# Performance work log

Measured on AMD Instinct MI355X. Metric: run time of the kernel, lower is better.

## Reference

```python
import jax, jax.numpy as jnp
import numpy as np

B, N = 32, 14            # hardcoded in the torch module
IN_F, OUT_F, H = 1024, 1024, 4
ALPHA = 0.2              # leaky relu negative slope
NEG = -9e15


def setup_inputs() -> dict:
    key = jax.random.key(0)
    ks = jax.random.split(key, 6)
    # xavier-uniform-ish scales (exact init values don't affect correctness testing)
    x = jax.random.normal(ks[0], (B, N, IN_F), dtype=jnp.float32)
    adj = jax.random.normal(ks[1], (B, N, N), dtype=jnp.float32)
    W = jax.random.normal(ks[2], (H, B, IN_F, OUT_F), dtype=jnp.float32) * (1.414 / np.sqrt(IN_F))
    a = jax.random.normal(ks[3], (H, B, 2 * OUT_F, 1), dtype=jnp.float32) * (1.414 / np.sqrt(2 * OUT_F))
    fc_w = jax.random.normal(ks[4], (H, OUT_F, N * OUT_F), dtype=jnp.float32) * (1.0 / np.sqrt(N * OUT_F))
    fc_b = jnp.zeros((H, OUT_F), dtype=jnp.float32)
    return {"x": x, "adj": adj, "W": W, "a": a, "fc_w": fc_w, "fc_b": fc_b}


def reference(x, adj, W, a, fc_w, fc_b):
    # Wh: [H, B, N, OUT_F]
    Wh = jnp.einsum('bni,hbio->hbno', x, W)
    a1 = a[:, :, :OUT_F, 0]   # [H, B, OUT_F]
    a2 = a[:, :, OUT_F:, 0]   # [H, B, OUT_F]
    Wh1 = jnp.einsum('hbno,hbo->hbn', Wh, a1)  # [H, B, N]
    Wh2 = jnp.einsum('hbno,hbo->hbn', Wh, a2)  # [H, B, N]
    e = jax.nn.leaky_relu(Wh1[..., :, None] + Wh2[..., None, :], negative_slope=ALPHA)  # [H,B,N,N]
    att = jnp.where(adj[None] > 0, e, NEG)
    # torch F.softmax(attention, dim=1) on [B,N,N] -> axis=2 here (first node axis)
    att = jax.nn.softmax(att, axis=2)
    # dropout p=0 (eval) -> no-op
    h_prime = jnp.einsum('hbnm,hbmo->hbno', att, Wh).reshape(H, B, N * OUT_F)
    out_h = jnp.einsum('hbf,hof->hbo', h_prime, fc_w) + fc_b[:, None, :]  # [H, B, OUT_F]
    out = out_h.sum(axis=0)                                              # [B, OUT_F]
    return jax.nn.log_softmax(out, axis=1)
```

## Files before the change

kernel.cpp:

```cpp
#include <hip/hip_runtime.h>
#include <hip/hip_bf16.h>

#define ALPHA 0.2f
#define NEGV  -9000000000000000.0f

typedef __attribute__((ext_vector_type(8))) short bf16x8;
typedef __attribute__((ext_vector_type(4))) float f32x4;

__device__ __forceinline__ short f2b(float f) {
  unsigned u = __float_as_uint(f);
  unsigned r = (u + 0x7FFFu + ((u >> 16) & 1u)) >> 16;
  return (short)r;
}

__global__ __launch_bounds__(256) void k1_wh(const float* __restrict__ x,
                                             const float* __restrict__ W,
                                             float* __restrict__ Wh) {
  int blk = blockIdx.x;
  int kc = blk & 3;
  int hb = blk >> 2;
  int b  = hb & 31;
  int t  = threadIdx.x;
  __shared__ float xs[14][256];
  int i0 = kc * 256;
  const float* xb = x + (size_t)b * 14 * 1024 + i0;
  #pragma unroll
  for (int n = 0; n < 14; ++n) xs[n][t] = xb[n * 1024 + t];
  __syncthreads();

  const float* Wp = W + ((size_t)hb * 1024 + i0) * 1024 + 4 * t;
  float4 acc[14];
  #pragma unroll
  for (int n = 0; n < 14; ++n) acc[n] = make_float4(0.f, 0.f, 0.f, 0.f);

  for (int ii = 0; ii < 256; ii += 4) {
    float4 w0 = *(const float4*)(Wp + (size_t)(ii + 0) * 1024);
    float4 w1 = *(const float4*)(Wp + (size_t)(ii + 1) * 1024);
    float4 w2 = *(const float4*)(Wp + (size_t)(ii + 2) * 1024);
    float4 w3 = *(const float4*)(Wp + (size_t)(ii + 3) * 1024);
    #pragma unroll
    for (int n = 0; n < 14; ++n) {
      float4 xn = *(const float4*)&xs[n][ii];
      acc[n].x += xn.x * w0.x + xn.y * w1.x + xn.z * w2.x + xn.w * w3.x;
      acc[n].y += xn.x * w0.y + xn.y * w1.y + xn.z * w2.y + xn.w * w3.y;
      acc[n].z += xn.x * w0.z + xn.y * w1.z + xn.z * w2.z + xn.w * w3.z;
      acc[n].w += xn.x * w0.w + xn.y * w1.w + xn.z * w2.w + xn.w * w3.w;
    }
  }

  float* dst = Wh + (size_t)hb * 14336 + 4 * t;
  #pragma unroll
  for (int n = 0; n < 14; ++n) {
    atomicAdd(dst + n * 1024 + 0, acc[n].x);
    atomicAdd(dst + n * 1024 + 1, acc[n].y);
    atomicAdd(dst + n * 1024 + 2, acc[n].z);
    atomicAdd(dst + n * 1024 + 3, acc[n].w);
  }
}

__global__ __launch_bounds__(64) void k2_att(const float* __restrict__ Wh,
                                             const float* __restrict__ adj,
                                             const float* __restrict__ a,
                                             float* __restrict__ att) {
  int hb = blockIdx.x;
  int b  = hb & 31;
  int l  = threadIdx.x;
  __shared__ float wh1s[14], wh2s[14];
  const float* whp = Wh + (size_t)hb * 14336;
  const float* a1  = a + (size_t)hb * 2048;
  const float* a2  = a1 + 1024;

  for (int n = 0; n < 14; ++n) {
    float p1 = 0.f, p2 = 0.f;
    #pragma unroll
    for (int j = 0; j < 16; ++j) {
      int o = l + 64 * j;
      float wv = whp[n * 1024 + o];
      p1 += wv * a1[o];
      p2 += wv * a2[o];
    }
    #pragma unroll
    for (int s = 32; s >= 1; s >>= 1) {
      p1 += __shfl_xor(p1, s);
      p2 += __shfl_xor(p2, s);
    }
    if (l == 0) { wh1s[n] = p1; wh2s[n] = p2; }
  }
  __syncthreads();

  if (l < 14) {
    int m = l;
    const float* adjb = adj + b * 196;
    float col[14];
    float mx = -1e30f;
    #pragma unroll
    for (int n = 0; n < 14; ++n) {
      float e = wh1s[n] + wh2s[m];
      e = (e > 0.f) ? e : ALPHA * e;
      e = (adjb[n * 14 + m] > 0.f) ? e : NEGV;
      col[n] = e;
      mx = fmaxf(mx, e);
    }
    float s = 0.f;
    #pragma unroll
    for (int n = 0; n < 14; ++n) { col[n] = expf(col[n] - mx); s += col[n]; }
    float inv = 1.f / s;
    #pragma unroll
    for (int n = 0; n < 14; ++n) att[hb * 196 + n * 14 + m] = col[n] * inv;
  }
}

__global__ __launch_bounds__(128) void k3_hprime(const float* __restrict__ Wh,
                                                 const float* __restrict__ att,
                                                 float* __restrict__ hp) {
  int blk = blockIdx.x;
  int hb = blk >> 1, oc = blk & 1;
  int t = threadIdx.x;
  __shared__ float att_s[196];
  for (int idx = t; idx < 196; idx += 128) att_s[idx] = att[hb * 196 + idx];
  __syncthreads();

  int o4 = oc * 512 + 4 * t;
  const float* whp = Wh + (size_t)hb * 14336;
  float4 acc[14];
  #pragma unroll
  for (int n = 0; n < 14; ++n) acc[n] = make_float4(0.f, 0.f, 0.f, 0.f);
  #pragma unroll
  for (int m = 0; m < 14; ++m) {
    float4 wm = *(const float4*)(whp + m * 1024 + o4);
    #pragma unroll
    for (int n = 0; n < 14; ++n) {
      float anm = att_s[n * 14 + m];
      acc[n].x += anm * wm.x;
      acc[n].y += anm * wm.y;
      acc[n].z += anm * wm.z;
      acc[n].w += anm * wm.w;
    }
  }
  float* dst = hp + (size_t)hb * 14336 + o4;
  #pragma unroll
  for (int n = 0; n < 14; ++n) *(float4*)(dst + n * 1024) = acc[n];
}

__global__ __launch_bounds__(256) void k4_fc(const float* __restrict__ hp,
                                             const float* __restrict__ fcw,
                                             float* __restrict__ oacc) {
  int blk = blockIdx.x;
  int kc = blk & 7;
  int oc = (blk >> 3) & 15;
  int h  = blk >> 7;
  int t = threadIdx.x;
  int lane = t & 63, w = t >> 6;
  int mw = w & 1, nw = w >> 1;
  __shared__ __align__(16) short As[32][272];
  __shared__ __align__(16) short Bs[64][272];
  const int o0 = oc * 64;
  const size_t hpb = (size_t)h * 32 * 14336;
  const size_t fwb = (size_t)h * 1024 * 14336;
  f32x4 c0 = {0.f, 0.f, 0.f, 0.f};
  f32x4 c1 = {0.f, 0.f, 0.f, 0.f};

  for (int tt = 0; tt < 7; ++tt) {
    int f0 = kc * 1792 + tt * 256;
    #pragma unroll
    for (int p = 0; p < 8; ++p) {
      int f4 = p * 256 + t;
      int row = f4 >> 6, c4 = f4 & 63;
      float4 wv = *(const float4*)(hp + hpb + (size_t)row * 14336 + f0 + 4 * c4);
      short4 s4 = make_short4(f2b(wv.x), f2b(wv.y), f2b(wv.z), f2b(wv.w));
      *(short4*)&As[row][4 * c4] = s4;
    }
    #pragma unroll
    for (int p = 0; p < 16; ++p) {
      int f4 = p * 256 + t;
      int row = f4 >> 6, c4 = f4 & 63;
      float4 wv = *(const float4*)(fcw + fwb + (size_t)(o0 + row) * 14336 + f0 + 4 * c4);
      short4 s4 = make_short4(f2b(wv.x), f2b(wv.y), f2b(wv.z), f2b(wv.w));
      *(short4*)&Bs[row][4 * c4] = s4;
    }
    __syncthreads();
    #pragma unroll
    for (int ks = 0; ks < 8; ++ks) {
      bf16x8 af = *(const bf16x8*)&As[mw * 16 + (lane & 15)][ks * 32 + (lane >> 4) * 8];
      bf16x8 b0 = *(const bf16x8*)&Bs[nw * 32 + (lane & 15)][ks * 32 + (lane >> 4) * 8];
      bf16x8 b1 = *(const bf16x8*)&Bs[nw * 32 + 16 + (lane & 15)][ks * 32 + (lane >> 4) * 8];
      c0 = __builtin_amdgcn_mfma_f32_16x16x32_bf16(af, b0, c0, 0, 0, 0);
      c1 = __builtin_amdgcn_mfma_f32_16x16x32_bf16(af, b1, c1, 0, 0, 0);
    }
    __syncthreads();
  }
  int br   = mw * 16 + (lane >> 4) * 4;
  int ocol = o0 + nw * 32 + (lane & 15);
  #pragma unroll
  for (int r = 0; r < 4; ++r) {
    atomicAdd(&oacc[(br + r) * 1024 + ocol],      c0[r]);
    atomicAdd(&oacc[(br + r) * 1024 + ocol + 16], c1[r]);
  }
}

__global__ __launch_bounds__(256) void k5_lsm(const float* __restrict__ oacc,
                                              const float* __restrict__ fcb,
                                              float* __restrict__ out) {
  int b = blockIdx.x, t = threadIdx.x;
  int lane = t & 63, wid = t >> 6;
  __shared__ float redm[4], reds[4];
  float v[4];
  float mx = -1e30f;
  #pragma unroll
  for (int j = 0; j < 4; ++j) {
    int o = t + 256 * j;
    float val = oacc[b * 1024 + o] + fcb[o] + fcb[1024 + o] + fcb[2048 + o] + fcb[3072 + o];
    v[j] = val;
    mx = fmaxf(mx, val);
  }
  #pragma unroll
  for (int s = 32; s >= 1; s >>= 1) mx = fmaxf(mx, __shfl_xor(mx, s));
  if (lane == 0) redm[wid] = mx;
  __syncthreads();
  mx = fmaxf(fmaxf(redm[0], redm[1]), fmaxf(redm[2], redm[3]));
  float sm = 0.f;
  #pragma unroll
  for (int j = 0; j < 4; ++j) sm += expf(v[j] - mx);
  #pragma unroll
  for (int s = 32; s >= 1; s >>= 1) sm += __shfl_xor(sm, s);
  if (lane == 0) reds[wid] = sm;
  __syncthreads();
  sm = reds[0] + reds[1] + reds[2] + reds[3];
  float lse = mx + logf(sm);
  #pragma unroll
  for (int j = 0; j < 4; ++j) {
    int o = t + 256 * j;
    out[b * 1024 + o] = v[j] - lse;
  }
}

extern "C" void kernel_launch(void* const* d_in, const int* in_sizes, int n_in,
                              void* d_out, int out_size, void* d_ws, size_t ws_size,
                              hipStream_t stream) {
  const float* x   = (const float*)d_in[0];
  const float* adj = (const float*)d_in[1];
  const float* W   = (const float*)d_in[2];
  const float* a   = (const float*)d_in[3];
  const float* fcw = (const float*)d_in[4];
  const float* fcb = (const float*)d_in[5];
  float* out = (float*)d_out;

  char* ws = (char*)d_ws;
  float* Wh  = (float*)(ws);
  float* att = (float*)(ws + 7340032);
  float* hp  = (float*)(ws + 7440384);
  float* oac = (float*)(ws + 14780416);

  hipMemsetAsync(Wh, 0, 7340032, stream);
  hipMemsetAsync(oac, 0, 131072, stream);

  k1_wh<<<512, 256, 0, stream>>>(x, W, Wh);
  k2_att<<<128, 64, 0, stream>>>(Wh, adj, a, att);
  k3_hprime<<<256, 128, 0, stream>>>(Wh, att, hp);
  k4_fc<<<512, 256, 0, stream>>>(hp, fcw, oac);
  k5_lsm<<<32, 256, 0, stream>>>(oac, fcb, out);
}
```

Before: 962.9 us.

## Replace split-K atomics with partial buffers and separate reduction passes

The k1 and k4 split-K kernels now write partial results to separate workspace slices instead of doing fp32 atomicAdd. A new k1b_red kernel and an extended k5 loop sum those partials. The two hipMemsetAsync calls are dropped. k2_att now uses two waves to compute the per-node attention dot products. This removes atomic contention and memset launches, at the cost of about 29 MB of extra partial traffic and one more kernel launch.

```diff
diff --git a/kernel.cpp b/kernel.cpp
--- a/kernel.cpp
+++ b/kernel.cpp
@@ -15,7 +15,7 @@
 
 __global__ __launch_bounds__(256) void k1_wh(const float* __restrict__ x,
                                              const float* __restrict__ W,
-                                             float* __restrict__ Wh) {
+                                             float* __restrict__ Whp) {
   int blk = blockIdx.x;
   int kc = blk & 3;
   int hb = blk >> 2;
@@ -48,29 +48,41 @@
     }
   }
 
-  float* dst = Wh + (size_t)hb * 14336 + 4 * t;
-  #pragma unroll
-  for (int n = 0; n < 14; ++n) {
-    atomicAdd(dst + n * 1024 + 0, acc[n].x);
-    atomicAdd(dst + n * 1024 + 1, acc[n].y);
-    atomicAdd(dst + n * 1024 + 2, acc[n].z);
-    atomicAdd(dst + n * 1024 + 3, acc[n].w);
-  }
-}
-
-__global__ __launch_bounds__(64) void k2_att(const float* __restrict__ Wh,
-                                             const float* __restrict__ adj,
-                                             const float* __restrict__ a,
-                                             float* __restrict__ att) {
+  float* dst = Whp + (size_t)kc * 1835008 + (size_t)hb * 14336 + 4 * t;
+  #pragma unroll
+  for (int n = 0; n < 14; ++n) *(float4*)(dst + n * 1024) = acc[n];
+}
+
+__global__ __launch_bounds__(256) void k1b_red(const float* __restrict__ p,
+                                               float* __restrict__ Wh) {
+  size_t idx = ((size_t)blockIdx.x * 256 + threadIdx.x) * 4;
+  const size_t S = 1835008;
+  float4 a = *(const float4*)(p + idx);
+  float4 b = *(const float4*)(p + S + idx);
+  float4 c = *(const float4*)(p + 2 * S + idx);
+  float4 d = *(const float4*)(p + 3 * S + idx);
+  a.x += b.x + c.x + d.x;
+  a.y += b.y + c.y + d.y;
+  a.z += b.z + c.z + d.z;
+  a.w += b.w + c.w + d.w;
+  *(float4*)(Wh + idx) = a;
+}
+
+__global__ __launch_bounds__(128) void k2_att(const float* __restrict__ Wh,
+                                              const float* __restrict__ adj,
+                                              const float* __restrict__ a,
+                                              float* __restrict__ att) {
   int hb = blockIdx.x;
   int b  = hb & 31;
-  int l  = threadIdx.x;
+  int t  = threadIdx.x;
+  int l  = t & 63, w = t >> 6;
   __shared__ float wh1s[14], wh2s[14];
   const float* whp = Wh + (size_t)hb * 14336;
   const float* a1  = a + (size_t)hb * 2048;
   const float* a2  = a1 + 1024;
 
-  for (int n = 0; n < 14; ++n) {
+  for (int nn = 0; nn < 7; ++nn) {
+    int n = w * 7 + nn;
     float p1 = 0.f, p2 = 0.f;
     #pragma unroll
     for (int j = 0; j < 16; ++j) {
@@ -88,8 +100,8 @@
   }
   __syncthreads();
 
-  if (l < 14) {
-    int m = l;
+  if (t < 14) {
+    int m = t;
     const float* adjb = adj + b * 196;
     float col[14];
     float mx = -1e30f;
@@ -144,7 +156,7 @@
 
 __global__ __launch_bounds__(256) void k4_fc(const float* __restrict__ hp,
                                              const float* __restrict__ fcw,
-                                             float* __restrict__ oacc) {
+                                             float* __restrict__ oaccp) {
   int blk = blockIdx.x;
   int kc = blk & 7;
   int oc = (blk >> 3) & 15;
@@ -189,16 +201,17 @@
     }
     __syncthreads();
   }
+  float* op = oaccp + (size_t)(kc * 4 + h) * 32768;
   int br   = mw * 16 + (lane >> 4) * 4;
   int ocol = o0 + nw * 32 + (lane & 15);
   #pragma unroll
   for (int r = 0; r < 4; ++r) {
-    atomicAdd(&oacc[(br + r) * 1024 + ocol],      c0[r]);
-    atomicAdd(&oacc[(br + r) * 1024 + ocol + 16], c1[r]);
-  }
-}
-
-__global__ __launch_bounds__(256) void k5_lsm(const float* __restrict__ oacc,
+    op[(br + r) * 1024 + ocol]      = c0[r];
+    op[(br + r) * 1024 + ocol + 16] = c1[r];
+  }
+}
+
+__global__ __launch_bounds__(256) void k5_lsm(const float* __restrict__ oaccp,
                                               const float* __restrict__ fcb,
                                               float* __restrict__ out) {
   int b = blockIdx.x, t = threadIdx.x;
@@ -209,7 +222,9 @@
   #pragma unroll
   for (int j = 0; j < 4; ++j) {
     int o = t + 256 * j;
-    float val = oacc[b * 1024 + o] + fcb[o] + fcb[1024 + o] + fcb[2048 + o] + fcb[3072 + o];
+    float val = fcb[o] + fcb[1024 + o] + fcb[2048 + o] + fcb[3072 + o];
+    #pragma unroll
+    for (int p = 0; p < 32; ++p) val += oaccp[(size_t)p * 32768 + b * 1024 + o];
     v[j] = val;
     mx = fmaxf(mx, val);
   }
@@ -246,17 +261,16 @@
   float* out = (float*)d_out;
 
   char* ws = (char*)d_ws;
-  float* Wh  = (float*)(ws);
-  float* att = (float*)(ws + 7340032);
-  float* hp  = (float*)(ws + 7440384);
-  float* oac = (float*)(ws + 14780416);
-
-  hipMemsetAsync(Wh, 0, 7340032, stream);
-  hipMemsetAsync(oac, 0, 131072, stream);
-
-  k1_wh<<<512, 256, 0, stream>>>(x, W, Wh);
-  k2_att<<<128, 64, 0, stream>>>(Wh, adj, a, att);
+  float* Whp = (float*)(ws);
+  float* Wh  = (float*)(ws + 29360128);
+  float* att = (float*)(ws + 36700160);
+  float* hp  = (float*)(ws + 36800512);
+  float* oap = (float*)(ws + 44140544);
+
+  k1_wh<<<512, 256, 0, stream>>>(x, W, Whp);
+  k1b_red<<<1792, 256, 0, stream>>>(Whp, Wh);
+  k2_att<<<128, 128, 0, stream>>>(Wh, adj, a, att);
   k3_hprime<<<256, 128, 0, stream>>>(Wh, att, hp);
-  k4_fc<<<512, 256, 0, stream>>>(hp, fcw, oac);
-  k5_lsm<<<32, 256, 0, stream>>>(oac, fcb, out);
-}
+  k4_fc<<<512, 256, 0, stream>>>(hp, fcw, oap);
+  k5_lsm<<<32, 256, 0, stream>>>(oap, fcb, out);
+}
```

Measured after the change: 895.1 us. 1.08x faster.
